# Kernel tuning notes

Measured on AMD Instinct MI355X. Metric: run time of the kernel, lower is better.

The kernel has to match this reference:

```python
import jax, jax.numpy as jnp
import numpy as np

N_NODES = 50000
N_EDGES = 800000
F_IN = 128
HID = 128
N_GRAPHS = 256


def setup_inputs() -> dict:
    key = jax.random.key(0)
    ks = jax.random.split(key, 12)
    gx = jax.random.normal(ks[0], (N_NODES, F_IN), dtype=jnp.float32)
    edge_index = jax.random.randint(ks[1], (2, N_EDGES), 0, N_NODES, dtype=jnp.int64)
    batch = jnp.sort(jax.random.randint(ks[2], (N_NODES,), 0, N_GRAPHS, dtype=jnp.int64))
    edge_attr = jax.random.uniform(ks[3], (N_EDGES,), dtype=jnp.float32)
    s1 = 1.0 / np.sqrt(F_IN)
    s2 = 1.0 / np.sqrt(HID)
    W1 = jax.random.uniform(ks[4], (F_IN, HID), jnp.float32, -s1, s1)
    b1 = jnp.zeros((HID,), jnp.float32)
    W2 = jax.random.uniform(ks[5], (HID, HID), jnp.float32, -s2, s2)
    b2 = jnp.zeros((HID,), jnp.float32)
    W3 = jax.random.uniform(ks[6], (HID, HID), jnp.float32, -s2, s2)
    b3 = jnp.zeros((HID,), jnp.float32)
    return {"gx": gx, "edge_index": edge_index, "batch": batch, "edge_attr": edge_attr,
            "W1": W1, "b1": b1, "W2": W2, "b2": b2, "W3": W3, "b3": b3}


def _gcn_conv(x, W, b, row, col, edge_weight, n_nodes):
    # PyG GCNConv with add_self_loops=False:
    #   deg[i] = sum of edge_weight over edges with dst == i
    #   norm_e = deg^{-1/2}[row] * w_e * deg^{-1/2}[col]
    #   out[i] = sum_{e: col_e == i} norm_e * (x @ W)[row_e] + b
    deg = jax.ops.segment_sum(edge_weight, col, num_segments=n_nodes)
    dinv = jnp.where(deg > 0, jax.lax.rsqrt(deg), 0.0)
    norm = dinv[row] * edge_weight * dinv[col]  # [E]
    h = x @ W  # [N, H]
    msg = h[row] * norm[:, None]  # [E, H] gather + scale
    out = jax.ops.segment_sum(msg, col, num_segments=n_nodes)  # scatter-add
    return out + b


def reference(gx, edge_index, batch, edge_attr, W1, b1, W2, b2, W3, b3):
    row, col = edge_index[0], edge_index[1]
    n = gx.shape[0]
    # dropout layers are in eval mode (identity) for a deterministic reference
    h = jax.nn.relu(_gcn_conv(gx, W1, b1, row, col, edge_attr, n))
    h = jax.nn.relu(_gcn_conv(h, W2, b2, row, col, edge_attr, n))
    h = _gcn_conv(h, W3, b3, row, col, edge_attr, n)
    readout = jax.ops.segment_sum(h, batch, num_segments=N_GRAPHS)  # global_add_pool
    return h, readout
```

## Files before the change

kernel.cpp:

```cpp
#include <hip/hip_runtime.h>

#define FEAT 128

typedef __attribute__((ext_vector_type(8))) short short8;
typedef __attribute__((ext_vector_type(4))) float f32x4;

__device__ __forceinline__ unsigned int bf16rtn(float f) {
    unsigned int u = __float_as_uint(f);
    return (u + 0x7fffu + ((u >> 16) & 1u)) >> 16;
}
__device__ __forceinline__ float bf16tof(unsigned int h) { return __uint_as_float(h << 16); }
__device__ __forceinline__ float bf16lo(unsigned int v) { return __uint_as_float(v << 16); }
__device__ __forceinline__ float bf16hi(unsigned int v) { return __uint_as_float(v & 0xffff0000u); }

__global__ __launch_bounds__(256) void prep_kernel(const float* __restrict__ W0,
                                                   const float* __restrict__ W1,
                                                   const float* __restrict__ W2,
                                                   unsigned short* __restrict__ Whi,
                                                   unsigned short* __restrict__ Wlo,
                                                   float* __restrict__ wdeg, int N) {
    const int t = threadIdx.x, x = blockIdx.x, y = blockIdx.y;
    if (y == 3) {
        int i = x * 256 + t;
        if (i < N) wdeg[i] = 0.f;
        return;
    }
    if (x >= 64) return;
    int i = x * 256 + t;
    const float* W = (y == 0) ? W0 : (y == 1) ? W1 : W2;
    int c = i >> 7, k = i & 127;
    float w = W[(size_t)k * FEAT + c];
    unsigned int h = bf16rtn(w);
    size_t off = (size_t)y * 16384 + (size_t)c * FEAT + k;
    Whi[off] = (unsigned short)h;
    Wlo[off] = (unsigned short)bf16rtn(w - bf16tof(h));
}

__global__ __launch_bounds__(256) void hist_kernel(const int* __restrict__ col,
                                                   const float* __restrict__ ew,
                                                   int* __restrict__ ghist,
                                                   float* __restrict__ wdeg,
                                                   int E, int nblk, int nbuck) {
    __shared__ int h[256];
    const int t = threadIdx.x, b = blockIdx.x;
    h[t] = 0;
    __syncthreads();
    const int base = b * 4096;
#pragma unroll
    for (int i = 0; i < 16; ++i) {
        int e = base + i * 256 + t;
        if (e < E) {
            int c = col[e];
            atomicAdd(&h[c >> 8], 1);
            atomicAdd(&wdeg[c], ew[e]);
        }
    }
    __syncthreads();
    if (t < nbuck) ghist[t * nblk + b] = h[t];
}

__global__ __launch_bounds__(256) void scan_block_kernel(const int* __restrict__ cnt,
                                                         int* __restrict__ out,
                                                         int* __restrict__ bsum, int M) {
    __shared__ int s[256];
    int t = threadIdx.x;
    int i = blockIdx.x * 256 + t;
    int own = (i < M) ? cnt[i] : 0;
    s[t] = own;
    for (int off = 1; off < 256; off <<= 1) {
        __syncthreads();
        int v = (t >= off) ? s[t - off] : 0;
        __syncthreads();
        s[t] += v;
    }
    __syncthreads();
    if (i < M) out[i] = s[t] - own;
    if (t == 255) bsum[blockIdx.x] = s[255];
}

__global__ __launch_bounds__(256) void scan_bsum_dinv_kernel(int* __restrict__ bsum, int nb,
                                                             const float* __restrict__ wdeg,
                                                             float* __restrict__ dinv, int N) {
    __shared__ int s[256];
    const int t = threadIdx.x, b = blockIdx.x;
    if (b > 0) {
        int node = (b - 1) * 256 + t;
        if (node < N) {
            float w = wdeg[node];
            dinv[node] = (w > 0.f) ? rsqrtf(w) : 0.f;
        }
        return;
    }
    int own = (t < nb) ? bsum[t] : 0;
    s[t] = own;
    for (int off = 1; off < 256; off <<= 1) {
        __syncthreads();
        int v = (t >= off) ? s[t - off] : 0;
        __syncthreads();
        s[t] += v;
    }
    __syncthreads();
    if (t < nb) bsum[t] = s[t] - own;
}

__global__ __launch_bounds__(256) void scatter1_kernel(const int* __restrict__ row,
                                                       const int* __restrict__ col,
                                                       const float* __restrict__ ew,
                                                       const float* __restrict__ dinv,
                                                       const int* __restrict__ gsc,
                                                       const int* __restrict__ bsum,
                                                       uint2* __restrict__ bedge,
                                                       int E, int nblk, int nbuck) {
    __shared__ int cur[256];
    const int t = threadIdx.x, b = blockIdx.x;
    if (t < nbuck) {
        int idx = t * nblk + b;
        cur[t] = gsc[idx] + bsum[idx >> 8];
    }
    __syncthreads();
    const int base = b * 4096;
#pragma unroll
    for (int i = 0; i < 16; ++i) {
        int e = base + i * 256 + t;
        if (e < E) {
            int c = col[e];
            int r = row[e];
            float w = dinv[r] * ew[e] * dinv[c];
            int slot = atomicAdd(&cur[c >> 8], 1);
            bedge[slot] = make_uint2(((unsigned)c << 16) | (unsigned)r, __float_as_uint(w));
        }
    }
}

__global__ __launch_bounds__(256) void bucket_kernel(const uint2* __restrict__ bedge,
                                                     const int* __restrict__ gsc,
                                                     const int* __restrict__ bsum,
                                                     int* __restrict__ rowptr,
                                                     uint2* __restrict__ sedge,
                                                     int N, int E, int nblk, int nbuck) {
    __shared__ int lcnt[256];
    __shared__ int lscan[256];
    __shared__ int lcur[256];

    const int d = blockIdx.x, t = threadIdx.x;
    const int i0 = d * nblk;
    const int base = gsc[i0] + bsum[i0 >> 8];
    int end;
    if (d == nbuck - 1) end = E;
    else {
        const int i1 = (d + 1) * nblk;
        end = gsc[i1] + bsum[i1 >> 8];
    }

    lcnt[t] = 0;
    __syncthreads();
    for (int i = base + t; i < end; i += 256) {
        uint2 p = bedge[i];
        atomicAdd(&lcnt[(p.x >> 16) & 255], 1);
    }
    __syncthreads();
    int own = lcnt[t];
    lscan[t] = own;
    for (int off = 1; off < 256; off <<= 1) {
        __syncthreads();
        int v = (t >= off) ? lscan[t - off] : 0;
        __syncthreads();
        lscan[t] += v;
    }
    __syncthreads();
    int excl = lscan[t] - own;
    lcur[t] = base + excl;
    int node = d * 256 + t;
    if (node < N) rowptr[node] = base + excl;
    if (d == nbuck - 1 && t == 0) rowptr[N] = E;
    __syncthreads();
    for (int i = base + t; i < end; i += 256) {
        uint2 p = bedge[i];
        int c = (p.x >> 16) & 255;
        int slot = atomicAdd(&lcur[c], 1);
        sedge[slot] = make_uint2(p.x & 0xFFFFu, p.y);
    }
}

__global__ __launch_bounds__(256) void gemm_mfma_kernel(
    const float* __restrict__ X,
    const unsigned short* __restrict__ Wthi, const unsigned short* __restrict__ Wtlo,
    unsigned int* __restrict__ hb,
    int N)
{
    __shared__ unsigned short wh[64 * 128];
    __shared__ unsigned short wl[64 * 128];

    const int tid = threadIdx.x;
    const int r0 = blockIdx.x * 64;
    const int cb = blockIdx.y;

#pragma unroll
    for (int it = 0; it < 4; ++it) {
        int idx = it * 256 + tid;
        int c = idx >> 4;
        int k8 = (idx & 15) * 8;
        int sw = k8 ^ ((c & 7) << 3);
        size_t src = (size_t)(cb * 64 + c) * FEAT + k8;
        *(short8*)&wh[c * 128 + sw] = *(const short8*)(Wthi + src);
        *(short8*)&wl[c * 128 + sw] = *(const short8*)(Wtlo + src);
    }
    __syncthreads();

    const int lane = tid & 63;
    const int wv = tid >> 6;
    const int m = lane & 15;
    const int quad = lane >> 4;
    const int arow = wv * 16 + m;
    const int grow = r0 + arow;
    const float* xrow = X + (size_t)grow * FEAT;

    f32x4 acc[4];
#pragma unroll
    for (int ct = 0; ct < 4; ++ct) acc[ct] = (f32x4){0.f, 0.f, 0.f, 0.f};

#pragma unroll
    for (int kt = 0; kt < 4; ++kt) {
        const int k0 = kt * 32 + quad * 8;
        float4 va = make_float4(0.f, 0.f, 0.f, 0.f);
        float4 vb = make_float4(0.f, 0.f, 0.f, 0.f);
        if (grow < N) {
            va = *(const float4*)(xrow + k0);
            vb = *(const float4*)(xrow + k0 + 4);
        }
        unsigned int h0 = bf16rtn(va.x), h1 = bf16rtn(va.y);
        unsigned int h2 = bf16rtn(va.z), h3 = bf16rtn(va.w);
        unsigned int h4 = bf16rtn(vb.x), h5 = bf16rtn(vb.y);
        unsigned int h6 = bf16rtn(vb.z), h7 = bf16rtn(vb.w);
        short8 ah, al;
        ah[0] = (short)h0; ah[1] = (short)h1; ah[2] = (short)h2; ah[3] = (short)h3;
        ah[4] = (short)h4; ah[5] = (short)h5; ah[6] = (short)h6; ah[7] = (short)h7;
        al[0] = (short)bf16rtn(va.x - bf16tof(h0));
        al[1] = (short)bf16rtn(va.y - bf16tof(h1));
        al[2] = (short)bf16rtn(va.z - bf16tof(h2));
        al[3] = (short)bf16rtn(va.w - bf16tof(h3));
        al[4] = (short)bf16rtn(vb.x - bf16tof(h4));
        al[5] = (short)bf16rtn(vb.y - bf16tof(h5));
        al[6] = (short)bf16rtn(vb.z - bf16tof(h6));
        al[7] = (short)bf16rtn(vb.w - bf16tof(h7));
#pragma unroll
        for (int ct = 0; ct < 4; ++ct) {
            int bc = ct * 16 + m;
            int bw = k0 ^ ((bc & 7) << 3);
            short8 bh = *(const short8*)&wh[bc * 128 + bw];
            short8 bl = *(const short8*)&wl[bc * 128 + bw];
            acc[ct] = __builtin_amdgcn_mfma_f32_16x16x32_bf16(ah, bh, acc[ct], 0, 0, 0);
            acc[ct] = __builtin_amdgcn_mfma_f32_16x16x32_bf16(ah, bl, acc[ct], 0, 0, 0);
            acc[ct] = __builtin_amdgcn_mfma_f32_16x16x32_bf16(al, bh, acc[ct], 0, 0, 0);
        }
    }

    __syncthreads();
    unsigned short* cl = wh;
#pragma unroll
    for (int ct = 0; ct < 4; ++ct)
#pragma unroll
        for (int reg = 0; reg < 4; ++reg) {
            int rrow = wv * 16 + quad * 4 + reg;
            cl[rrow * 72 + ct * 16 + m] = (unsigned short)bf16rtn(acc[ct][reg]);
        }
    __syncthreads();
#pragma unroll
    for (int it = 0; it < 2; ++it) {
        int idx = it * 256 + tid;
        int r = idx >> 3;
        int c4 = (idx & 7) * 4;
        int gr = r0 + r;
        if (gr < N) {
            uint4 pv = *(const uint4*)&cl[r * 72 + c4 * 2];
            *(uint4*)(hb + (size_t)gr * 64 + cb * 32 + c4) = pv;
        }
    }
}

template <int RELU>
__global__ __launch_bounds__(256) void agg_kernel(
    const int* __restrict__ rowptr, const uint2* __restrict__ sedge,
    const uint2* __restrict__ hb2,
    const float* __restrict__ bias,
    float* __restrict__ outX, int N)
{
    const int node = blockIdx.x * 4 + (threadIdx.x >> 6);
    if (node >= N) return;
    const int lane = threadIdx.x & 63;
    const int h = lane >> 5;
    const int j = lane & 31;
    const int s = rowptr[node];
    const int e = rowptr[node + 1];

    float a0 = 0.f, a1 = 0.f, a2 = 0.f, a3 = 0.f;

    for (int gb = s; gb < e; gb += 16) {
        uint2 m0, m1, m2, m3, m4, m5, m6, m7;
        if (gb + 16 <= e) {
            m0 = sedge[gb + 0 + h];  m1 = sedge[gb + 2 + h];
            m2 = sedge[gb + 4 + h];  m3 = sedge[gb + 6 + h];
            m4 = sedge[gb + 8 + h];  m5 = sedge[gb + 10 + h];
            m6 = sedge[gb + 12 + h]; m7 = sedge[gb + 14 + h];
        } else {
            const uint2 z = make_uint2(0u, 0u);
            int i0 = gb + 0 + h, i1 = gb + 2 + h, i2 = gb + 4 + h, i3 = gb + 6 + h;
            int i4 = gb + 8 + h, i5 = gb + 10 + h, i6 = gb + 12 + h, i7 = gb + 14 + h;
            m0 = (i0 < e) ? sedge[i0] : z;  m1 = (i1 < e) ? sedge[i1] : z;
            m2 = (i2 < e) ? sedge[i2] : z;  m3 = (i3 < e) ? sedge[i3] : z;
            m4 = (i4 < e) ? sedge[i4] : z;  m5 = (i5 < e) ? sedge[i5] : z;
            m6 = (i6 < e) ? sedge[i6] : z;  m7 = (i7 < e) ? sedge[i7] : z;
        }
        uint2 v0 = hb2[(size_t)m0.x * 32 + j];
        uint2 v1 = hb2[(size_t)m1.x * 32 + j];
        uint2 v2 = hb2[(size_t)m2.x * 32 + j];
        uint2 v3 = hb2[(size_t)m3.x * 32 + j];
        uint2 v4 = hb2[(size_t)m4.x * 32 + j];
        uint2 v5 = hb2[(size_t)m5.x * 32 + j];
        uint2 v6 = hb2[(size_t)m6.x * 32 + j];
        uint2 v7 = hb2[(size_t)m7.x * 32 + j];
        float w0 = __uint_as_float(m0.y), w1 = __uint_as_float(m1.y);
        float w2 = __uint_as_float(m2.y), w3 = __uint_as_float(m3.y);
        float w4 = __uint_as_float(m4.y), w5 = __uint_as_float(m5.y);
        float w6 = __uint_as_float(m6.y), w7 = __uint_as_float(m7.y);
        a0 = fmaf(w0, bf16lo(v0.x), a0); a1 = fmaf(w0, bf16hi(v0.x), a1);
        a2 = fmaf(w0, bf16lo(v0.y), a2); a3 = fmaf(w0, bf16hi(v0.y), a3);
        a0 = fmaf(w1, bf16lo(v1.x), a0); a1 = fmaf(w1, bf16hi(v1.x), a1);
        a2 = fmaf(w1, bf16lo(v1.y), a2); a3 = fmaf(w1, bf16hi(v1.y), a3);
        a0 = fmaf(w2, bf16lo(v2.x), a0); a1 = fmaf(w2, bf16hi(v2.x), a1);
        a2 = fmaf(w2, bf16lo(v2.y), a2); a3 = fmaf(w2, bf16hi(v2.y), a3);
        a0 = fmaf(w3, bf16lo(v3.x), a0); a1 = fmaf(w3, bf16hi(v3.x), a1);
        a2 = fmaf(w3, bf16lo(v3.y), a2); a3 = fmaf(w3, bf16hi(v3.y), a3);
        a0 = fmaf(w4, bf16lo(v4.x), a0); a1 = fmaf(w4, bf16hi(v4.x), a1);
        a2 = fmaf(w4, bf16lo(v4.y), a2); a3 = fmaf(w4, bf16hi(v4.y), a3);
        a0 = fmaf(w5, bf16lo(v5.x), a0); a1 = fmaf(w5, bf16hi(v5.x), a1);
        a2 = fmaf(w5, bf16lo(v5.y), a2); a3 = fmaf(w5, bf16hi(v5.y), a3);
        a0 = fmaf(w6, bf16lo(v6.x), a0); a1 = fmaf(w6, bf16hi(v6.x), a1);
        a2 = fmaf(w6, bf16lo(v6.y), a2); a3 = fmaf(w6, bf16hi(v6.y), a3);
        a0 = fmaf(w7, bf16lo(v7.x), a0); a1 = fmaf(w7, bf16hi(v7.x), a1);
        a2 = fmaf(w7, bf16lo(v7.y), a2); a3 = fmaf(w7, bf16hi(v7.y), a3);
    }

    a0 += __shfl_xor(a0, 32);
    a1 += __shfl_xor(a1, 32);
    a2 += __shfl_xor(a2, 32);
    a3 += __shfl_xor(a3, 32);

    if (h == 0) {
        float4 bv = ((const float4*)bias)[j];
        a0 += bv.x; a1 += bv.y; a2 += bv.z; a3 += bv.w;
        if (RELU) {
            a0 = fmaxf(a0, 0.f); a1 = fmaxf(a1, 0.f);
            a2 = fmaxf(a2, 0.f); a3 = fmaxf(a3, 0.f);
        }
        *(float4*)(outX + (size_t)node * FEAT + j * 4) = make_float4(a0, a1, a2, a3);
    }
}

__global__ __launch_bounds__(256) void readout_kernel(const float* __restrict__ h,
                                                      const int* __restrict__ batch,
                                                      float* __restrict__ ro, int N) {
    __shared__ float part[128];
    const int g = blockIdx.x;
    const int j = threadIdx.x & 127;
    const int half = threadIdx.x >> 7;
    int lo = 0, hi = N;
    while (lo < hi) { int mid = (lo + hi) >> 1; if (batch[mid] < g) lo = mid + 1; else hi = mid; }
    int lo2 = lo, hi2 = N;
    while (lo2 < hi2) { int mid = (lo2 + hi2) >> 1; if (batch[mid] < g + 1) lo2 = mid + 1; else hi2 = mid; }

    float s0 = 0.f, s1 = 0.f;
    int n = lo + half;
    for (; n + 2 < lo2; n += 4) {
        s0 += h[(size_t)n * FEAT + j];
        s1 += h[(size_t)(n + 2) * FEAT + j];
    }
    if (n < lo2) s0 += h[(size_t)n * FEAT + j];
    float s = s0 + s1;
    if (half == 1) part[j] = s;
    __syncthreads();
    if (half == 0) ro[(size_t)g * FEAT + j] = s + part[j];
}

static inline size_t align256(size_t x) { return (x + 255) & ~(size_t)255; }

extern "C" void kernel_launch(void* const* d_in, const int* in_sizes, int n_in,
                              void* d_out, int out_size, void* d_ws, size_t ws_size,
                              hipStream_t stream) {
    const float* gx    = (const float*)d_in[0];
    const int*   ei    = (const int*)d_in[1];
    const int*   batch = (const int*)d_in[2];
    const float* ew    = (const float*)d_in[3];
    const float* W1 = (const float*)d_in[4];
    const float* b1 = (const float*)d_in[5];
    const float* W2 = (const float*)d_in[6];
    const float* b2 = (const float*)d_in[7];
    const float* W3 = (const float*)d_in[8];
    const float* b3 = (const float*)d_in[9];

    const int N = in_sizes[0] / FEAT;
    const int E = in_sizes[3];
    const int G = (out_size - N * FEAT) / FEAT;

    const int* row = ei;
    const int* col = ei + E;

    const int nbuck = (N + 255) >> 8;
    const int nblk  = (E + 4095) >> 12;
    const int M     = nbuck * nblk;

    char* ws = (char*)d_ws;
    int*   rowptr = (int*)ws;         ws += align256((size_t)(N + 1) * 4);
    float* dinv   = (float*)ws;       ws += align256((size_t)N * 4);
    int*   ghist  = (int*)ws;         ws += align256((size_t)M * 4);
    int*   gsc    = (int*)ws;         ws += align256((size_t)M * 4);
    int*   bsum   = (int*)ws;         ws += align256(256 * 4);
    uint2* bedge  = (uint2*)ws;       ws += align256((size_t)E * 8);
    uint2* sedge  = (uint2*)ws;       ws += align256((size_t)E * 8);
    unsigned int* hb = (unsigned int*)ws;  ws += align256((size_t)N * 64 * 4);
    float* bufX   = (float*)ws;       ws += align256((size_t)N * FEAT * 4);
    unsigned short* Wh = (unsigned short*)ws; ws += align256((size_t)3 * 16384 * 2);
    unsigned short* Wl = (unsigned short*)ws; ws += align256((size_t)3 * 16384 * 2);

    float* wdeg = bufX;

    float* h_out = (float*)d_out;
    float* ro    = h_out + (size_t)N * FEAT;

    const int pgx = max((N + 255) / 256, 64);
    prep_kernel<<<dim3(pgx, 4), 256, 0, stream>>>(W1, W2, W3, Wh, Wl, wdeg, N);

    hist_kernel<<<nblk, 256, 0, stream>>>(col, ew, ghist, wdeg, E, nblk, nbuck);
    const int snb = (M + 255) / 256;
    scan_block_kernel<<<snb, 256, 0, stream>>>(ghist, gsc, bsum, M);
    scan_bsum_dinv_kernel<<<1 + nbuck, 256, 0, stream>>>(bsum, snb, wdeg, dinv, N);
    scatter1_kernel<<<nblk, 256, 0, stream>>>(row, col, ew, dinv, gsc, bsum, bedge, E, nblk, nbuck);
    bucket_kernel<<<nbuck, 256, 0, stream>>>(bedge, gsc, bsum, rowptr, sedge, N, E, nblk, nbuck);

    dim3 ggrid((N + 63) / 64, 2);
    const int ablocks = (N + 3) / 4;
    const uint2* hb2 = (const uint2*)hb;

    gemm_mfma_kernel<<<ggrid, 256, 0, stream>>>(gx, Wh, Wl, hb, N);
    agg_kernel<1><<<ablocks, 256, 0, stream>>>(rowptr, sedge, hb2, b1, bufX, N);
    gemm_mfma_kernel<<<ggrid, 256, 0, stream>>>(bufX, Wh + 16384, Wl + 16384, hb, N);
    agg_kernel<1><<<ablocks, 256, 0, stream>>>(rowptr, sedge, hb2, b2, bufX, N);
    gemm_mfma_kernel<<<ggrid, 256, 0, stream>>>(bufX, Wh + 32768, Wl + 32768, hb, N);
    agg_kernel<0><<<ablocks, 256, 0, stream>>>(rowptr, sedge, hb2, b3, h_out, N);
    readout_kernel<<<G, 256, 0, stream>>>(h_out, batch, ro, N);
}
```

Baseline: 331.0 us.

## Compute degree in bucket kernel via shared atomics, add separate edge-norm pass

The weighted in-degree is no longer accumulated with global float atomics in the histogram pass. It is now summed with shared-memory atomics inside the per-bucket sort kernel, which also computes dinv there and multiplies each edge weight by the destination-side dinv. A new norm_kernel then applies the source-side dinv[row] in a separate pass over the sorted edges, and the weight conversion moves into its own kernel. This trades about 800k contended global atomics for one extra read-modify-write pass over the edge array and one extra launch.

```diff
diff --git a/kernel.cpp b/kernel.cpp
--- a/kernel.cpp
+++ b/kernel.cpp
@@ -13,33 +13,8 @@
 __device__ __forceinline__ float bf16lo(unsigned int v) { return __uint_as_float(v << 16); }
 __device__ __forceinline__ float bf16hi(unsigned int v) { return __uint_as_float(v & 0xffff0000u); }
 
-__global__ __launch_bounds__(256) void prep_kernel(const float* __restrict__ W0,
-                                                   const float* __restrict__ W1,
-                                                   const float* __restrict__ W2,
-                                                   unsigned short* __restrict__ Whi,
-                                                   unsigned short* __restrict__ Wlo,
-                                                   float* __restrict__ wdeg, int N) {
-    const int t = threadIdx.x, x = blockIdx.x, y = blockIdx.y;
-    if (y == 3) {
-        int i = x * 256 + t;
-        if (i < N) wdeg[i] = 0.f;
-        return;
-    }
-    if (x >= 64) return;
-    int i = x * 256 + t;
-    const float* W = (y == 0) ? W0 : (y == 1) ? W1 : W2;
-    int c = i >> 7, k = i & 127;
-    float w = W[(size_t)k * FEAT + c];
-    unsigned int h = bf16rtn(w);
-    size_t off = (size_t)y * 16384 + (size_t)c * FEAT + k;
-    Whi[off] = (unsigned short)h;
-    Wlo[off] = (unsigned short)bf16rtn(w - bf16tof(h));
-}
-
 __global__ __launch_bounds__(256) void hist_kernel(const int* __restrict__ col,
-                                                   const float* __restrict__ ew,
                                                    int* __restrict__ ghist,
-                                                   float* __restrict__ wdeg,
                                                    int E, int nblk, int nbuck) {
     __shared__ int h[256];
     const int t = threadIdx.x, b = blockIdx.x;
@@ -49,11 +24,7 @@
 #pragma unroll
     for (int i = 0; i < 16; ++i) {
         int e = base + i * 256 + t;
-        if (e < E) {
-            int c = col[e];
-            atomicAdd(&h[c >> 8], 1);
-            atomicAdd(&wdeg[c], ew[e]);
-        }
+        if (e < E) atomicAdd(&h[col[e] >> 8], 1);
     }
     __syncthreads();
     if (t < nbuck) ghist[t * nblk + b] = h[t];
@@ -78,19 +49,9 @@
     if (t == 255) bsum[blockIdx.x] = s[255];
 }
 
-__global__ __launch_bounds__(256) void scan_bsum_dinv_kernel(int* __restrict__ bsum, int nb,
-                                                             const float* __restrict__ wdeg,
-                                                             float* __restrict__ dinv, int N) {
+__global__ __launch_bounds__(256) void scan_bsum_kernel(int* __restrict__ bsum, int nb) {
     __shared__ int s[256];
-    const int t = threadIdx.x, b = blockIdx.x;
-    if (b > 0) {
-        int node = (b - 1) * 256 + t;
-        if (node < N) {
-            float w = wdeg[node];
-            dinv[node] = (w > 0.f) ? rsqrtf(w) : 0.f;
-        }
-        return;
-    }
+    int t = threadIdx.x;
     int own = (t < nb) ? bsum[t] : 0;
     s[t] = own;
     for (int off = 1; off < 256; off <<= 1) {
@@ -106,7 +67,6 @@
 __global__ __launch_bounds__(256) void scatter1_kernel(const int* __restrict__ row,
                                                        const int* __restrict__ col,
                                                        const float* __restrict__ ew,
-                                                       const float* __restrict__ dinv,
                                                        const int* __restrict__ gsc,
                                                        const int* __restrict__ bsum,
                                                        uint2* __restrict__ bedge,
@@ -124,10 +84,9 @@
         int e = base + i * 256 + t;
         if (e < E) {
             int c = col[e];
-            int r = row[e];
-            float w = dinv[r] * ew[e] * dinv[c];
             int slot = atomicAdd(&cur[c >> 8], 1);
-            bedge[slot] = make_uint2(((unsigned)c << 16) | (unsigned)r, __float_as_uint(w));
+            bedge[slot] = make_uint2(((unsigned)c << 16) | (unsigned)row[e],
+                                     __float_as_uint(ew[e]));
         }
     }
 }
@@ -136,11 +95,14 @@
                                                      const int* __restrict__ gsc,
                                                      const int* __restrict__ bsum,
                                                      int* __restrict__ rowptr,
+                                                     float* __restrict__ dinv,
                                                      uint2* __restrict__ sedge,
                                                      int N, int E, int nblk, int nbuck) {
     __shared__ int lcnt[256];
+    __shared__ float lw[256];
     __shared__ int lscan[256];
     __shared__ int lcur[256];
+    __shared__ float ldv[256];
 
     const int d = blockIdx.x, t = threadIdx.x;
     const int i0 = d * nblk;
@@ -153,10 +115,13 @@
     }
 
     lcnt[t] = 0;
+    lw[t] = 0.f;
     __syncthreads();
     for (int i = base + t; i < end; i += 256) {
         uint2 p = bedge[i];
-        atomicAdd(&lcnt[(p.x >> 16) & 255], 1);
+        int c = (p.x >> 16) & 255;
+        atomicAdd(&lcnt[c], 1);
+        atomicAdd(&lw[c], __uint_as_float(p.y));
     }
     __syncthreads();
     int own = lcnt[t];
@@ -170,16 +135,46 @@
     __syncthreads();
     int excl = lscan[t] - own;
     lcur[t] = base + excl;
+    float wsum = lw[t];
+    float dv = (wsum > 0.f) ? rsqrtf(wsum) : 0.f;
+    ldv[t] = dv;
     int node = d * 256 + t;
-    if (node < N) rowptr[node] = base + excl;
+    if (node < N) {
+        rowptr[node] = base + excl;
+        dinv[node] = dv;
+    }
     if (d == nbuck - 1 && t == 0) rowptr[N] = E;
     __syncthreads();
     for (int i = base + t; i < end; i += 256) {
         uint2 p = bedge[i];
         int c = (p.x >> 16) & 255;
         int slot = atomicAdd(&lcur[c], 1);
-        sedge[slot] = make_uint2(p.x & 0xFFFFu, p.y);
-    }
+        sedge[slot] = make_uint2(p.x & 0xFFFFu,
+                                 __float_as_uint(__uint_as_float(p.y) * ldv[c]));
+    }
+}
+
+__global__ void norm_kernel(uint2* __restrict__ sedge, const float* __restrict__ dinv, int E) {
+    int i = blockIdx.x * blockDim.x + threadIdx.x;
+    if (i < E) {
+        uint2 p = sedge[i];
+        p.y = __float_as_uint(__uint_as_float(p.y) * dinv[p.x]);
+        sedge[i] = p;
+    }
+}
+
+__global__ void convw_kernel(const float* __restrict__ W0, const float* __restrict__ W1,
+                             const float* __restrict__ W2,
+                             unsigned short* __restrict__ Whi, unsigned short* __restrict__ Wlo) {
+    int i = blockIdx.x * blockDim.x + threadIdx.x;
+    int which = blockIdx.y;
+    const float* W = (which == 0) ? W0 : (which == 1) ? W1 : W2;
+    int c = i >> 7, k = i & 127;
+    float w = W[(size_t)k * FEAT + c];
+    unsigned int h = bf16rtn(w);
+    size_t off = (size_t)which * 16384 + (size_t)c * FEAT + k;
+    Whi[off] = (unsigned short)h;
+    Wlo[off] = (unsigned short)bf16rtn(w - bf16tof(h));
 }
 
 __global__ __launch_bounds__(256) void gemm_mfma_kernel(
@@ -422,20 +417,18 @@
     unsigned short* Wh = (unsigned short*)ws; ws += align256((size_t)3 * 16384 * 2);
     unsigned short* Wl = (unsigned short*)ws; ws += align256((size_t)3 * 16384 * 2);
 
-    float* wdeg = bufX;
-
     float* h_out = (float*)d_out;
     float* ro    = h_out + (size_t)N * FEAT;
 
-    const int pgx = max((N + 255) / 256, 64);
-    prep_kernel<<<dim3(pgx, 4), 256, 0, stream>>>(W1, W2, W3, Wh, Wl, wdeg, N);
-
-    hist_kernel<<<nblk, 256, 0, stream>>>(col, ew, ghist, wdeg, E, nblk, nbuck);
+    hist_kernel<<<nblk, 256, 0, stream>>>(col, ghist, E, nblk, nbuck);
     const int snb = (M + 255) / 256;
     scan_block_kernel<<<snb, 256, 0, stream>>>(ghist, gsc, bsum, M);
-    scan_bsum_dinv_kernel<<<1 + nbuck, 256, 0, stream>>>(bsum, snb, wdeg, dinv, N);
-    scatter1_kernel<<<nblk, 256, 0, stream>>>(row, col, ew, dinv, gsc, bsum, bedge, E, nblk, nbuck);
-    bucket_kernel<<<nbuck, 256, 0, stream>>>(bedge, gsc, bsum, rowptr, sedge, N, E, nblk, nbuck);
+    scan_bsum_kernel<<<1, 256, 0, stream>>>(bsum, snb);
+    scatter1_kernel<<<nblk, 256, 0, stream>>>(row, col, ew, gsc, bsum, bedge, E, nblk, nbuck);
+    bucket_kernel<<<nbuck, 256, 0, stream>>>(bedge, gsc, bsum, rowptr, dinv, sedge, N, E, nblk, nbuck);
+    norm_kernel<<<(E + 255) / 256, 256, 0, stream>>>(sedge, dinv, E);
+
+    convw_kernel<<<dim3(64, 3), 256, 0, stream>>>(W1, W2, W3, Wh, Wl);
 
     dim3 ggrid((N + 63) / 64, 2);
     const int ablocks = (N + 3) / 4;
```

New measurement: 298.8 us. 1.11x faster.
